# Kernel tuning notes

Hardware: AMD Instinct MI355X
Metric: run time of the kernel (lower is better)

Reference implementation:

```python
import jax, jax.numpy as jnp
import numpy as np

NUM_HEADS = 12
HEAD_DIM = 64
DIM = 768


def _rot_interleaved(t):
    # rot(x): pairs (x0,x1) -> (-x1, x0), interleaved layout
    x1 = t[..., ::2]
    x2 = t[..., 1::2]
    return jnp.stack([-x2, x1], axis=-1).reshape(t.shape)


def _apply_rope_cat(t, emb):
    # emb: [N, 2*head_dim] = concat(sin, cos); t: [B, H, N, head_dim]
    sin_e, cos_e = jnp.split(emb, 2, axis=-1)  # each [N, head_dim]
    return t * cos_e + _rot_interleaved(t) * sin_e


def setup_inputs() -> dict:
    key = jax.random.key(0)
    ks = jax.random.split(key, 8)
    B, Nq, Nkv = 16, 256, 4096
    s = 1.0 / np.sqrt(DIM)
    return {
        "x": jax.random.normal(ks[0], (B, Nq, DIM), dtype=jnp.float32),
        "context": jax.random.normal(ks[1], (B, Nkv, DIM), dtype=jnp.float32),
        "rope_q": jax.random.normal(ks[2], (Nq, 2 * HEAD_DIM), dtype=jnp.float32),
        "rope_k": jax.random.normal(ks[3], (Nkv, 2 * HEAD_DIM), dtype=jnp.float32),
        "Wq": jax.random.normal(ks[4], (DIM, DIM), dtype=jnp.float32) * s,
        "Wk": jax.random.normal(ks[5], (DIM, DIM), dtype=jnp.float32) * s,
        "Wv": jax.random.normal(ks[6], (DIM, DIM), dtype=jnp.float32) * s,
        "Wo": jax.random.normal(ks[7], (DIM, DIM), dtype=jnp.float32) * s,
    }


def reference(x, context, rope_q, rope_k, Wq, Wk, Wv, Wo):
    B, Nq, _ = x.shape
    Nkv = context.shape[1]
    H, hd = NUM_HEADS, HEAD_DIM
    scale = hd ** -0.5

    # projections -> [B, H, N, hd]
    q = jnp.einsum('bnd,df->bnf', x, Wq).reshape(B, Nq, H, hd).transpose(0, 2, 1, 3)
    k = jnp.einsum('bnd,df->bnf', context, Wk).reshape(B, Nkv, H, hd).transpose(0, 2, 1, 3)
    v = jnp.einsum('bnd,df->bnf', context, Wv).reshape(B, Nkv, H, hd).transpose(0, 2, 1, 3)

    q = _apply_rope_cat(q, rope_q)
    k = _apply_rope_cat(k, rope_k)

    attn = jnp.einsum('bhqd,bhkd->bhqk', q * scale, k)
    attn = jax.nn.softmax(attn, axis=-1)
    o = jnp.einsum('bhqk,bhkd->bhqd', attn, v)  # [B, H, Nq, hd]
    o = o.transpose(0, 2, 1, 3).reshape(B, Nq, H * hd)
    return jnp.einsum('bnf,fo->bno', o, Wo)
```

## Files before the change

### kernel.cpp

```cpp
#include <hip/hip_runtime.h>
#include <stdint.h>


typedef __bf16 bf16x8 __attribute__((ext_vector_type(8)));
typedef unsigned short u16x8 __attribute__((ext_vector_type(8)));
typedef unsigned short u16x4 __attribute__((ext_vector_type(4)));
typedef uint32_t u32x4 __attribute__((ext_vector_type(4)));
typedef float f32x4 __attribute__((ext_vector_type(4)));

#define DIMF 768
#define NHEAD 12
#define NKV 4096
#define NQ 256
#define NB 16

struct alignas(8) us4 { unsigned short x, y, z, w; };

__device__ __forceinline__ unsigned short f2bf(float x) {
  uint32_t u = __float_as_uint(x);
  u += 0x7fffu + ((u >> 16) & 1u);
  return (unsigned short)(u >> 16);
}

__device__ __forceinline__ uint32_t cvtpk(float a, float b) {
  uint32_t r;
  asm("v_cvt_pk_bf16_f32 %0, %1, %2" : "=v"(r) : "v"(a), "v"(b));
  return r;
}

__device__ __forceinline__ void gld_lds16(const unsigned short* g, unsigned short* l) {
  __builtin_amdgcn_global_load_lds(
      (const __attribute__((address_space(1))) uint32_t*)(uintptr_t)g,
      (__attribute__((address_space(3))) uint32_t*)(uintptr_t)l, 16, 0, 0);
}

__global__ void cvt_kernel(const float* __restrict__ in, unsigned short* __restrict__ out, int n) {
  int stride = gridDim.x * blockDim.x * 4;
  for (int i = (blockIdx.x * blockDim.x + threadIdx.x) * 4; i < n; i += stride) {
    float4 v = *(const float4*)(in + i);
    us4 o{f2bf(v.x), f2bf(v.y), f2bf(v.z), f2bf(v.w)};
    *(us4*)(out + i) = o;
  }
}

__global__ void twt_kernel(const float* __restrict__ W0, const float* __restrict__ W1,
                           const float* __restrict__ W2, const float* __restrict__ W3,
                           unsigned short* __restrict__ O0, unsigned short* __restrict__ O1,
                           unsigned short* __restrict__ O2, unsigned short* __restrict__ O3) {
  const float* W; unsigned short* O;
  switch (blockIdx.z) {
    case 0: W = W0; O = O0; break;
    case 1: W = W1; O = O1; break;
    case 2: W = W2; O = O2; break;
    default: W = W3; O = O3; break;
  }
  __shared__ float t[32][33];
  int x0 = blockIdx.x * 32, y0 = blockIdx.y * 32;
  int tx = threadIdx.x, ty = threadIdx.y;
#pragma unroll
  for (int j = 0; j < 4; ++j)
    t[ty + 8 * j][tx] = W[(size_t)(y0 + ty + 8 * j) * DIMF + x0 + tx];
  __syncthreads();
#pragma unroll
  for (int j = 0; j < 4; ++j)
    O[(size_t)(x0 + ty + 8 * j) * DIMF + y0 + tx] = f2bf(t[tx][ty + 8 * j]);
}

__launch_bounds__(512, 2)
__global__ void kv8_kernel(const unsigned short* __restrict__ A,
                           const unsigned short* __restrict__ Bkv,
                           unsigned short* __restrict__ Ko,
                           unsigned short* __restrict__ Vt,
                           const float* __restrict__ rope) {
  extern __shared__ unsigned short smem[];
  const int t = threadIdx.x;
  const int lane = t & 63, wid = t >> 6;
  const int g = lane >> 4, lc = lane & 15;
  const int wr = wid >> 2, wc = wid & 3;

  const int swz = (blockIdx.x & 7) * 192 + (blockIdx.x >> 3);
  const int rowBase = (swz / 6) * 256;
  const int colBase = (swz % 6) * 256;

  f32x4 acc[8][4];
#pragma unroll
  for (int m = 0; m < 8; ++m)
#pragma unroll
    for (int n = 0; n < 4; ++n)
#pragma unroll
      for (int r = 0; r < 4; ++r) acc[m][n][r] = 0.f;

  const int sr = lane >> 3;
  const int sc = (lane & 7) ^ sr;
  const unsigned short* Abase0 = A + (size_t)(rowBase + wid * 16 + sr) * DIMF + sc * 8;
  const unsigned short* Bbase0 = Bkv + (size_t)(colBase + wid * 16 + sr) * DIMF + sc * 8;

#define STAGE_A(T, h)                                                              \
  do {                                                                             \
    unsigned short* _lb = smem + (((T) & 1) * 2 + (h)) * 8192;                     \
    const unsigned short* _gb = Abase0 + (size_t)(h) * 128 * DIMF + (T) * 64;      \
    gld_lds16(_gb, _lb + (wid * 16) * 64);                                         \
    gld_lds16(_gb + (size_t)8 * DIMF, _lb + (wid * 16 + 8) * 64);                  \
  } while (0)
#define STAGE_B(T, h)                                                              \
  do {                                                                             \
    unsigned short* _lb = smem + 32768 + (((T) & 1) * 2 + (h)) * 8192;             \
    const unsigned short* _gb = Bbase0 + (size_t)(h) * 128 * DIMF + (T) * 64;      \
    gld_lds16(_gb, _lb + (wid * 16) * 64);                                         \
    gld_lds16(_gb + (size_t)8 * DIMF, _lb + (wid * 16 + 8) * 64);                  \
  } while (0)

  STAGE_A(0, 0); STAGE_B(0, 0); STAGE_B(0, 1); STAGE_A(0, 1);
  STAGE_A(1, 0); STAGE_B(1, 0);

  bf16x8 af[4][2], bfr[2][2];

  for (int T = 0; T < 12; ++T) {
    const int dbuf = T & 1;
    if (T == 11) asm volatile("s_waitcnt vmcnt(0)" ::: "memory");
    else         asm volatile("s_waitcnt vmcnt(4)" ::: "memory");
    asm volatile("" ::: "memory");
    __builtin_amdgcn_s_barrier();
    asm volatile("" ::: "memory");

#pragma unroll
    for (int q = 0; q < 4; ++q) {
      const int ah = q >> 1, bh = q & 1;
      const unsigned short* Ab = smem + (dbuf * 2 + ah) * 8192;
      const unsigned short* Bb = smem + 32768 + (dbuf * 2 + bh) * 8192;
      if ((q & 1) == 0) {
#pragma unroll
        for (int mp = 0; mp < 4; ++mp)
#pragma unroll
          for (int kk = 0; kk < 2; ++kk) {
            int row = mp * 32 + wr * 16 + lc;
            af[mp][kk] = *(const bf16x8*)&Ab[row * 64 + (((kk * 4 + g) ^ (row & 7)) << 3)];
          }
      }
#pragma unroll
      for (int np = 0; np < 2; ++np)
#pragma unroll
        for (int kk = 0; kk < 2; ++kk) {
          int row = np * 64 + wc * 16 + lc;
          bfr[np][kk] = *(const bf16x8*)&Bb[row * 64 + (((kk * 4 + g) ^ (row & 7)) << 3)];
        }
      if (q == 0)      { if (T + 1 < 12) STAGE_B(T + 1, 1); }
      else if (q == 1) { if (T + 1 < 12) STAGE_A(T + 1, 1); }
      else if (q == 2) { if (T + 2 < 12) STAGE_A(T + 2, 0); }
      else             { if (T + 2 < 12) STAGE_B(T + 2, 0); }
      asm volatile("" ::: "memory");
      __builtin_amdgcn_s_barrier();
      asm volatile("s_waitcnt lgkmcnt(0)" ::: "memory");
      __builtin_amdgcn_s_setprio(1);
#pragma unroll
      for (int mp = 0; mp < 4; ++mp)
#pragma unroll
        for (int np = 0; np < 2; ++np)
#pragma unroll
          for (int kk = 0; kk < 2; ++kk)
            acc[4 * ah + mp][2 * bh + np] = __builtin_amdgcn_mfma_f32_16x16x32_bf16(
                af[mp][kk], bfr[np][kk], acc[4 * ah + mp][2 * bh + np], 0, 0, 0);
      __builtin_amdgcn_s_setprio(0);
      asm volatile("" ::: "memory");
      __builtin_amdgcn_s_barrier();
    }
  }
#undef STAGE_A
#undef STAGE_B

  if (colBase < 768) {
#pragma unroll
    for (int m = 0; m < 8; ++m)
#pragma unroll
      for (int n = 0; n < 4; ++n)
#pragma unroll
        for (int r = 0; r < 4; ++r) {
          int p = rowBase + m * 32 + wr * 16 + g * 4 + r;
          int f = colBase + n * 64 + wc * 16 + lc;
          int d = f & 63, h = f >> 6;
          float v = acc[m][n][r];
          float vo = __shfl_xor(v, 1);
          int b = p >> 12, nkv = p & 4095;
          float sn = rope[nkv * 128 + d], cs = rope[nkv * 128 + 64 + d];
          float o = (d & 1) ? fmaf(vo, sn, v * cs) : fmaf(-vo, sn, v * cs);
          Ko[((size_t)(b * NHEAD + h) * NKV + nkv) * 64 + d] = f2bf(o);
        }
  } else {
#pragma unroll
    for (int m = 0; m < 8; ++m)
#pragma unroll
      for (int n = 0; n < 4; ++n) {
        int p0 = rowBase + m * 32 + wr * 16 + g * 4;
        int b = p0 >> 12, nkv0 = p0 & 4095;
        int f = (colBase - 768) + n * 64 + wc * 16 + lc;
        int d = f & 63, h = f >> 6;
        us4 wv{f2bf(acc[m][n][0]), f2bf(acc[m][n][1]), f2bf(acc[m][n][2]), f2bf(acc[m][n][3])};
        *(us4*)&Vt[((size_t)(b * NHEAD + h) * 64 + d) * NKV + nkv0] = wv;
      }
  }
}

template <int MODE>
__launch_bounds__(256, 2)
__global__ void gemm_kernel(const unsigned short* __restrict__ A,
                            const unsigned short* __restrict__ Bt,
                            void* __restrict__ outp,
                            const float* __restrict__ rope) {
  __shared__ unsigned short As[128 * 64];
  __shared__ unsigned short Bs[128 * 64];
  const int t = threadIdx.x;
  const int lane = t & 63, wid = t >> 6;
  const int g = lane >> 4, lc = lane & 15;
  const int wr = wid >> 1, wc = wid & 1;
  const int rowBase = blockIdx.x * 128, colBase = blockIdx.y * 128;

  const f32x4 z4 = {0.f, 0.f, 0.f, 0.f};
  f32x4 acc[4][4];
#pragma unroll
  for (int m = 0; m < 4; ++m)
#pragma unroll
    for (int n = 0; n < 4; ++n) acc[m][n] = z4;

  const int r0 = t >> 3;
  const int c0 = t & 7;

  bf16x8 ra[4], rbx[4];
#pragma unroll
  for (int pp = 0; pp < 4; ++pp) {
    int row = pp * 32 + r0;
    ra[pp] = *(const bf16x8*)(A + (size_t)(rowBase + row) * DIMF + c0 * 8);
    rbx[pp] = *(const bf16x8*)(Bt + (size_t)(colBase + row) * DIMF + c0 * 8);
  }

  for (int kb = 0; kb < 12; ++kb) {
    __syncthreads();
#pragma unroll
    for (int pp = 0; pp < 4; ++pp) {
      int row = pp * 32 + r0;
      int ph = ((c0 ^ (row & 7)) << 3);
      *(bf16x8*)&As[row * 64 + ph] = ra[pp];
      *(bf16x8*)&Bs[row * 64 + ph] = rbx[pp];
    }
    __syncthreads();
    if (kb + 1 < 12) {
      int kn = (kb + 1) * 64;
#pragma unroll
      for (int pp = 0; pp < 4; ++pp) {
        int row = pp * 32 + r0;
        ra[pp] = *(const bf16x8*)(A + (size_t)(rowBase + row) * DIMF + kn + c0 * 8);
        rbx[pp] = *(const bf16x8*)(Bt + (size_t)(colBase + row) * DIMF + kn + c0 * 8);
      }
    }
#pragma unroll
    for (int kk = 0; kk < 2; ++kk) {
      bf16x8 af[4], bfr[4];
#pragma unroll
      for (int m = 0; m < 4; ++m) {
        int row = wr * 64 + m * 16 + lc;
        int ch = kk * 4 + g;
        af[m] = *(const bf16x8*)&As[row * 64 + (((ch ^ (row & 7))) << 3)];
      }
#pragma unroll
      for (int n = 0; n < 4; ++n) {
        int row = wc * 64 + n * 16 + lc;
        int ch = kk * 4 + g;
        bfr[n] = *(const bf16x8*)&Bs[row * 64 + (((ch ^ (row & 7))) << 3)];
      }
#pragma unroll
      for (int m = 0; m < 4; ++m)
#pragma unroll
        for (int n = 0; n < 4; ++n)
          acc[m][n] = __builtin_amdgcn_mfma_f32_16x16x32_bf16(af[m], bfr[n], acc[m][n], 0, 0, 0);
    }
  }

  if (MODE == 2) {
    unsigned short* Ko = (unsigned short*)outp;
#pragma unroll
    for (int m = 0; m < 4; ++m)
#pragma unroll
      for (int n = 0; n < 4; ++n)
#pragma unroll
        for (int r = 0; r < 4; ++r) {
          int p = rowBase + wr * 64 + m * 16 + g * 4 + r;
          int f = colBase + wc * 64 + n * 16 + lc;
          int d = f & 63, h = f >> 6;
          float v = acc[m][n][r];
          float vo = __shfl_xor(v, 1);
          int b = p >> 8, nq = p & 255;
          float sn = rope[nq * 128 + d], cs = rope[nq * 128 + 64 + d];
          float o = (d & 1) ? fmaf(vo, sn, v * cs) : fmaf(-vo, sn, v * cs);
          Ko[((size_t)(b * NHEAD + h) * NQ + nq) * 64 + d] = f2bf(o * 0.125f);
        }
  } else {
    float* Co = (float*)outp;
#pragma unroll
    for (int m = 0; m < 4; ++m)
#pragma unroll
      for (int n = 0; n < 4; ++n)
#pragma unroll
        for (int r = 0; r < 4; ++r) {
          int p = rowBase + wr * 64 + m * 16 + g * 4 + r;
          int f = colBase + wc * 64 + n * 16 + lc;
          Co[(size_t)p * DIMF + f] = acc[m][n][r];
        }
  }
}

__launch_bounds__(256, 2)
__global__ void attn_kernel(const unsigned short* __restrict__ Qb,
                            const unsigned short* __restrict__ Kb,
                            const unsigned short* __restrict__ Vtb,
                            unsigned short* __restrict__ Ob) {
  __shared__ unsigned short Ks[128 * 64];
  __shared__ unsigned short Vts[64 * 128];
  const int logical = (blockIdx.x & 7) * 96 + (blockIdx.x >> 3);
  const int qt = logical & 3, bh = logical >> 2;
  const int b = bh / NHEAD, h = bh % NHEAD;
  const int t = threadIdx.x;
  const int lane = t & 63, w = t >> 6;
  const int g = lane >> 4, lc = lane & 15;
  const int qrow = qt * 64 + w * 16 + lc;

  bf16x8 qf[2];
#pragma unroll
  for (int kk = 0; kk < 2; ++kk)
    qf[kk] = *(const bf16x8*)(Qb + ((size_t)bh * NQ + qrow) * 64 + kk * 32 + g * 8);

  const f32x4 z4 = {0.f, 0.f, 0.f, 0.f};
  f32x4 oacc[4];
#pragma unroll
  for (int df = 0; df < 4; ++df) oacc[df] = z4;
  float mrun = -1e30f, lrun = 0.f;

  const int r0 = t >> 3, c0 = t & 7;
  const int d0 = t >> 4, cv = t & 15;
  const int pbase = 32 * (cv >> 2) + 16 * (cv & 1) + 4 * ((cv >> 1) & 1);
  const int ch0 = pbase >> 3, of0 = pbase & 7;
  const int ch1 = (pbase + 8) >> 3;

  u16x8 rk[4], rv[4];
#define LOAD_TILE(KT)                                                                        \
  do {                                                                                       \
    const int kvb = (KT) * 128;                                                              \
    _Pragma("unroll")                                                                        \
    for (int pp = 0; pp < 4; ++pp)                                                           \
      rk[pp] = *(const u16x8*)(Kb + ((size_t)bh * NKV + kvb + pp * 32 + r0) * 64 + c0 * 8);  \
    _Pragma("unroll")                                                                        \
    for (int pp = 0; pp < 4; ++pp)                                                           \
      rv[pp] = *(const u16x8*)(Vtb + ((size_t)bh * 64 + pp * 16 + d0) * NKV + kvb + cv * 8); \
  } while (0)

  LOAD_TILE(0);

  for (int kt = 0; kt < 32; ++kt) {
    __syncthreads();
#pragma unroll
    for (int pp = 0; pp < 4; ++pp) {
      int row = pp * 32 + r0;
      *(u16x8*)&Ks[row * 64 + ((c0 ^ (row & 7)) << 3)] = rk[pp];
    }
#pragma unroll
    for (int pp = 0; pp < 4; ++pp) {
      int d = pp * 16 + d0;
      u16x4 lo = __builtin_shufflevector(rv[pp], rv[pp], 0, 1, 2, 3);
      u16x4 hi = __builtin_shufflevector(rv[pp], rv[pp], 4, 5, 6, 7);
      *(u16x4*)&Vts[d * 128 + ((ch0 ^ (d & 15)) << 3) + of0] = lo;
      *(u16x4*)&Vts[d * 128 + ((ch1 ^ (d & 15)) << 3) + of0] = hi;
    }
    if (kt + 1 < 32) LOAD_TILE(kt + 1);
    __syncthreads();

    f32x4 s[8];
#pragma unroll
    for (int c = 0; c < 8; ++c) s[c] = z4;
#pragma unroll
    for (int kk = 0; kk < 2; ++kk)
#pragma unroll
      for (int c = 0; c < 8; ++c) {
        int row = c * 16 + lc;
        bf16x8 kf = *(const bf16x8*)&Ks[row * 64 + (((kk * 4 + g) ^ (row & 7)) << 3)];
        s[c] = __builtin_amdgcn_mfma_f32_16x16x32_bf16(kf, qf[kk], s[c], 0, 0, 0);
      }

    float mx = s[0][0];
#pragma unroll
    for (int c = 0; c < 8; ++c)
#pragma unroll
      for (int r = 0; r < 4; ++r) mx = fmaxf(mx, s[c][r]);
    mx = fmaxf(mx, __shfl_xor(mx, 16));
    mx = fmaxf(mx, __shfl_xor(mx, 32));
    float nm = fmaxf(mrun, mx);
    float al = __expf(mrun - nm);
    mrun = nm;
    float ls = 0.f;
#pragma unroll
    for (int c = 0; c < 8; ++c)
#pragma unroll
      for (int r = 0; r < 4; ++r) {
        float p = __expf(s[c][r] - nm);
        s[c][r] = p;
        ls += p;
      }
    ls += __shfl_xor(ls, 16);
    ls += __shfl_xor(ls, 32);
    lrun = lrun * al + ls;
#pragma unroll
    for (int df = 0; df < 4; ++df)
#pragma unroll
      for (int r = 0; r < 4; ++r) oacc[df][r] *= al;

    uint32_t pk[8][2];
#pragma unroll
    for (int c = 0; c < 8; ++c)
#pragma unroll
      for (int w2 = 0; w2 < 2; ++w2)
        pk[c][w2] = cvtpk(s[c][2 * w2], s[c][2 * w2 + 1]);

#pragma unroll
    for (int kb = 0; kb < 4; ++kb) {
      u32x4 pw = {pk[2 * kb][0], pk[2 * kb][1], pk[2 * kb + 1][0], pk[2 * kb + 1][1]};
      bf16x8 pa = __builtin_bit_cast(bf16x8, pw);
#pragma unroll
      for (int df = 0; df < 4; ++df) {
        int row = df * 16 + lc;
        bf16x8 vf = *(const bf16x8*)&Vts[row * 128 + (((kb * 4 + g) ^ (row & 15)) << 3)];
        oacc[df] = __builtin_amdgcn_mfma_f32_16x16x32_bf16(vf, pa, oacc[df], 0, 0, 0);
      }
    }
  }
#undef LOAD_TILE

  float inv = 1.0f / lrun;
#pragma unroll
  for (int df = 0; df < 4; ++df) {
    us4 wv{f2bf(oacc[df][0] * inv), f2bf(oacc[df][1] * inv),
           f2bf(oacc[df][2] * inv), f2bf(oacc[df][3] * inv)};
    *(us4*)&Ob[((size_t)b * NQ + qrow) * DIMF + h * 64 + df * 16 + g * 4] = wv;
  }
}

extern "C" void kernel_launch(void* const* d_in, const int* in_sizes, int n_in,
                              void* d_out, int out_size, void* d_ws, size_t ws_size,
                              hipStream_t stream) {
  const float* x      = (const float*)d_in[0];
  const float* ctx    = (const float*)d_in[1];
  const float* rope_q = (const float*)d_in[2];
  const float* rope_k = (const float*)d_in[3];
  const float* Wq     = (const float*)d_in[4];
  const float* Wk     = (const float*)d_in[5];
  const float* Wv     = (const float*)d_in[6];
  const float* Wo     = (const float*)d_in[7];

  char* ws = (char*)d_ws;
  const size_t SZ_CTXB = (size_t)NB * NKV * DIMF * 2;
  const size_t SZ_XB   = (size_t)NB * NQ * DIMF * 2;
  const size_t SZ_WT   = (size_t)DIMF * DIMF * 2;
  unsigned short* ctxb = (unsigned short*)(ws);
  unsigned short* ob   = (unsigned short*)(ws);
  unsigned short* xb   = (unsigned short*)(ws + SZ_CTXB);
  unsigned short* wkt  = (unsigned short*)(ws + SZ_CTXB + SZ_XB);
  unsigned short* wvt  = (unsigned short*)(ws + SZ_CTXB + SZ_XB + SZ_WT);
  unsigned short* wqt  = (unsigned short*)(ws + SZ_CTXB + SZ_XB + 2 * SZ_WT);
  unsigned short* wot  = (unsigned short*)(ws + SZ_CTXB + SZ_XB + 3 * SZ_WT);
  unsigned short* kb   = (unsigned short*)(ws + SZ_CTXB + SZ_XB + 4 * SZ_WT);
  unsigned short* vtb  = (unsigned short*)(ws + SZ_CTXB + SZ_XB + 4 * SZ_WT + SZ_CTXB);
  unsigned short* qb   = (unsigned short*)(ws + SZ_CTXB + SZ_XB + 4 * SZ_WT + 2 * SZ_CTXB);

  cvt_kernel<<<dim3(2048), dim3(256), 0, stream>>>(ctx, ctxb, NB * NKV * DIMF);
  cvt_kernel<<<dim3(1024), dim3(256), 0, stream>>>(x, xb, NB * NQ * DIMF);
  twt_kernel<<<dim3(24, 24, 4), dim3(32, 8), 0, stream>>>(Wk, Wv, Wq, Wo, wkt, wvt, wqt, wot);

  kv8_kernel<<<dim3(1536), dim3(512), 131072, stream>>>(ctxb, wkt, kb, vtb, rope_k);
  gemm_kernel<2><<<dim3(32, 6), dim3(256), 0, stream>>>(xb, wqt, qb, rope_q);

  attn_kernel<<<dim3(768), dim3(256), 0, stream>>>(qb, kb, vtb, ob);

  gemm_kernel<3><<<dim3(32, 6), dim3(256), 0, stream>>>(ob, wot, d_out, nullptr);
}
```

Before: 390.6 us.

## Make KV projection GEMM persistent over column tiles with continuous K-pipeline

The KV projection kernel now launches 256 blocks, one per 256-row strip, and each block walks all six 256-wide output column tiles inside one flat 72-step loop. Global-to-LDS prefetch runs straight across tile boundaries, and the epilogue (RoPE for K, transposed store for V) runs in the middle of the loop. This removes the pipeline prologue and drain that each of the 1536 former blocks paid, and it reuses the A strip from L2. The cost is fewer blocks, 256 on a 256-CU part, so occupancy drops and any tail imbalance is exposed. The in-loop epilogue can also stall the prefetch stream.

```diff
diff --git a/kernel.cpp b/kernel.cpp
--- a/kernel.cpp
+++ b/kernel.cpp
@@ -67,20 +67,19 @@
 }
 
 __launch_bounds__(512, 2)
-__global__ void kv8_kernel(const unsigned short* __restrict__ A,
-                           const unsigned short* __restrict__ Bkv,
-                           unsigned short* __restrict__ Ko,
-                           unsigned short* __restrict__ Vt,
-                           const float* __restrict__ rope) {
+__global__ void kv8p_kernel(const unsigned short* __restrict__ A,
+                            const unsigned short* __restrict__ Bkv,
+                            unsigned short* __restrict__ Ko,
+                            unsigned short* __restrict__ Vt,
+                            const float* __restrict__ rope) {
   extern __shared__ unsigned short smem[];
   const int t = threadIdx.x;
   const int lane = t & 63, wid = t >> 6;
   const int g = lane >> 4, lc = lane & 15;
   const int wr = wid >> 2, wc = wid & 3;
 
-  const int swz = (blockIdx.x & 7) * 192 + (blockIdx.x >> 3);
-  const int rowBase = (swz / 6) * 256;
-  const int colBase = (swz % 6) * 256;
+  const int bidl = (blockIdx.x & 7) * 32 + (blockIdx.x >> 3);
+  const int rowBase = bidl * 256;
 
   f32x4 acc[8][4];
 #pragma unroll
@@ -93,32 +92,38 @@
   const int sr = lane >> 3;
   const int sc = (lane & 7) ^ sr;
   const unsigned short* Abase0 = A + (size_t)(rowBase + wid * 16 + sr) * DIMF + sc * 8;
-  const unsigned short* Bbase0 = Bkv + (size_t)(colBase + wid * 16 + sr) * DIMF + sc * 8;
-
-#define STAGE_A(T, h)                                                              \
+  const unsigned short* Bcol0  = Bkv + (size_t)(wid * 16 + sr) * DIMF + sc * 8;
+
+#define STAGE_A(KT, SLOT, H)                                                       \
   do {                                                                             \
-    unsigned short* _lb = smem + (((T) & 1) * 2 + (h)) * 8192;                     \
-    const unsigned short* _gb = Abase0 + (size_t)(h) * 128 * DIMF + (T) * 64;      \
+    unsigned short* _lb = smem + ((SLOT) * 2 + (H)) * 8192;                        \
+    const unsigned short* _gb = Abase0 + (size_t)(H) * 128 * DIMF + (KT) * 64;     \
     gld_lds16(_gb, _lb + (wid * 16) * 64);                                         \
     gld_lds16(_gb + (size_t)8 * DIMF, _lb + (wid * 16 + 8) * 64);                  \
   } while (0)
-#define STAGE_B(T, h)                                                              \
+#define STAGE_B(BB, KT, SLOT, H)                                                   \
   do {                                                                             \
-    unsigned short* _lb = smem + 32768 + (((T) & 1) * 2 + (h)) * 8192;             \
-    const unsigned short* _gb = Bbase0 + (size_t)(h) * 128 * DIMF + (T) * 64;      \
+    unsigned short* _lb = smem + 32768 + ((SLOT) * 2 + (H)) * 8192;                \
+    const unsigned short* _gb = (BB) + (size_t)(H) * 128 * DIMF + (KT) * 64;       \
     gld_lds16(_gb, _lb + (wid * 16) * 64);                                         \
     gld_lds16(_gb + (size_t)8 * DIMF, _lb + (wid * 16 + 8) * 64);                  \
   } while (0)
 
-  STAGE_A(0, 0); STAGE_B(0, 0); STAGE_B(0, 1); STAGE_A(0, 1);
-  STAGE_A(1, 0); STAGE_B(1, 0);
+  STAGE_A(0, 0, 0); STAGE_B(Bcol0, 0, 0, 0); STAGE_B(Bcol0, 0, 0, 1); STAGE_A(0, 0, 1);
+  STAGE_A(1, 1, 0); STAGE_B(Bcol0, 1, 1, 0);
+
+  int kt1 = 1, kt2 = 2;
+  const unsigned short* Bb1 = Bcol0;
+  const unsigned short* Bb2 = Bcol0;
+  int ktc = 0;
+  int colBase = 0;
 
   bf16x8 af[4][2], bfr[2][2];
 
-  for (int T = 0; T < 12; ++T) {
-    const int dbuf = T & 1;
-    if (T == 11) asm volatile("s_waitcnt vmcnt(0)" ::: "memory");
-    else         asm volatile("s_waitcnt vmcnt(4)" ::: "memory");
+  for (int gT = 0; gT < 72; ++gT) {
+    const int dbuf = gT & 1;
+    if (gT == 71) asm volatile("s_waitcnt vmcnt(0)" ::: "memory");
+    else          asm volatile("s_waitcnt vmcnt(4)" ::: "memory");
     asm volatile("" ::: "memory");
     __builtin_amdgcn_s_barrier();
     asm volatile("" ::: "memory");
@@ -144,10 +149,10 @@
           int row = np * 64 + wc * 16 + lc;
           bfr[np][kk] = *(const bf16x8*)&Bb[row * 64 + (((kk * 4 + g) ^ (row & 7)) << 3)];
         }
-      if (q == 0)      { if (T + 1 < 12) STAGE_B(T + 1, 1); }
-      else if (q == 1) { if (T + 1 < 12) STAGE_A(T + 1, 1); }
-      else if (q == 2) { if (T + 2 < 12) STAGE_A(T + 2, 0); }
-      else             { if (T + 2 < 12) STAGE_B(T + 2, 0); }
+      if (q == 0)      { if (gT < 71) STAGE_B(Bb1, kt1, dbuf ^ 1, 1); }
+      else if (q == 1) { if (gT < 71) STAGE_A(kt1, dbuf ^ 1, 1); }
+      else if (q == 2) { if (gT < 70) STAGE_A(kt2, dbuf, 0); }
+      else             { if (gT < 70) STAGE_B(Bb2, kt2, dbuf, 0); }
       asm volatile("" ::: "memory");
       __builtin_amdgcn_s_barrier();
       asm volatile("s_waitcnt lgkmcnt(0)" ::: "memory");
@@ -164,40 +169,56 @@
       asm volatile("" ::: "memory");
       __builtin_amdgcn_s_barrier();
     }
+
+    kt1 = kt2; Bb1 = Bb2;
+    ++kt2;
+    if (kt2 == 12) { kt2 = 0; Bb2 += (size_t)256 * DIMF; }
+
+    if (ktc == 11) {
+      if (colBase < 768) {
+#pragma unroll
+        for (int m = 0; m < 8; ++m)
+#pragma unroll
+          for (int n = 0; n < 4; ++n)
+#pragma unroll
+            for (int r = 0; r < 4; ++r) {
+              int p = rowBase + m * 32 + wr * 16 + g * 4 + r;
+              int f = colBase + n * 64 + wc * 16 + lc;
+              int d = f & 63, h = f >> 6;
+              float v = acc[m][n][r];
+              float vo = __shfl_xor(v, 1);
+              int b = p >> 12, nkv = p & 4095;
+              float sn = rope[nkv * 128 + d], cs = rope[nkv * 128 + 64 + d];
+              float o = (d & 1) ? fmaf(vo, sn, v * cs) : fmaf(-vo, sn, v * cs);
+              Ko[((size_t)(b * NHEAD + h) * NKV + nkv) * 64 + d] = f2bf(o);
+            }
+      } else {
+#pragma unroll
+        for (int m = 0; m < 8; ++m)
+#pragma unroll
+          for (int n = 0; n < 4; ++n) {
+            int p0 = rowBase + m * 32 + wr * 16 + g * 4;
+            int b = p0 >> 12, nkv0 = p0 & 4095;
+            int f = (colBase - 768) + n * 64 + wc * 16 + lc;
+            int d = f & 63, h = f >> 6;
+            us4 wv{f2bf(acc[m][n][0]), f2bf(acc[m][n][1]), f2bf(acc[m][n][2]), f2bf(acc[m][n][3])};
+            *(us4*)&Vt[((size_t)(b * NHEAD + h) * 64 + d) * NKV + nkv0] = wv;
+          }
+      }
+      colBase += 256;
+      ktc = 0;
+#pragma unroll
+      for (int m = 0; m < 8; ++m)
+#pragma unroll
+        for (int n = 0; n < 4; ++n)
+#pragma unroll
+          for (int r = 0; r < 4; ++r) acc[m][n][r] = 0.f;
+    } else {
+      ++ktc;
+    }
   }
 #undef STAGE_A
 #undef STAGE_B
-
-  if (colBase < 768) {
-#pragma unroll
-    for (int m = 0; m < 8; ++m)
-#pragma unroll
-      for (int n = 0; n < 4; ++n)
-#pragma unroll
-        for (int r = 0; r < 4; ++r) {
-          int p = rowBase + m * 32 + wr * 16 + g * 4 + r;
-          int f = colBase + n * 64 + wc * 16 + lc;
-          int d = f & 63, h = f >> 6;
-          float v = acc[m][n][r];
-          float vo = __shfl_xor(v, 1);
-          int b = p >> 12, nkv = p & 4095;
-          float sn = rope[nkv * 128 + d], cs = rope[nkv * 128 + 64 + d];
-          float o = (d & 1) ? fmaf(vo, sn, v * cs) : fmaf(-vo, sn, v * cs);
-          Ko[((size_t)(b * NHEAD + h) * NKV + nkv) * 64 + d] = f2bf(o);
-        }
-  } else {
-#pragma unroll
-    for (int m = 0; m < 8; ++m)
-#pragma unroll
-      for (int n = 0; n < 4; ++n) {
-        int p0 = rowBase + m * 32 + wr * 16 + g * 4;
-        int b = p0 >> 12, nkv0 = p0 & 4095;
-        int f = (colBase - 768) + n * 64 + wc * 16 + lc;
-        int d = f & 63, h = f >> 6;
-        us4 wv{f2bf(acc[m][n][0]), f2bf(acc[m][n][1]), f2bf(acc[m][n][2]), f2bf(acc[m][n][3])};
-        *(us4*)&Vt[((size_t)(b * NHEAD + h) * 64 + d) * NKV + nkv0] = wv;
-      }
-  }
 }
 
 template <int MODE>
@@ -471,7 +492,7 @@
   cvt_kernel<<<dim3(1024), dim3(256), 0, stream>>>(x, xb, NB * NQ * DIMF);
   twt_kernel<<<dim3(24, 24, 4), dim3(32, 8), 0, stream>>>(Wk, Wv, Wq, Wo, wkt, wvt, wqt, wot);
 
-  kv8_kernel<<<dim3(1536), dim3(512), 131072, stream>>>(ctxb, wkt, kb, vtb, rope_k);
+  kv8p_kernel<<<dim3(256), dim3(512), 131072, stream>>>(ctxb, wkt, kb, vtb, rope_k);
   gemm_kernel<2><<<dim3(32, 6), dim3(256), 0, stream>>>(xb, wqt, qb, rope_q);
 
   attn_kernel<<<dim3(768), dim3(256), 0, stream>>>(qb, kb, vtb, ob);
```

Result: slower. 417.1 us (+6.8%).
